# Performance work log

Measured on AMD Instinct MI355X. Metric: run time of the kernel, lower is better.

The kernel has to match this reference:

```python
import jax, jax.numpy as jnp
import numpy as np

META_DIM, CIN, COUT, K = 32, 64, 64, 3
B, N, S = 32, 256, 64


def setup_inputs() -> dict:
    key = jax.random.key(0)
    k1, k2, k3, k4, k5, k6 = jax.random.split(key, 6)
    scale = 1.0 / np.sqrt(META_DIM)
    return {
        "meta_knowledge": jax.random.normal(k1, (B, N, META_DIM), dtype=jnp.float32),
        "x": jax.random.normal(k2, (B, N, S, CIN), dtype=jnp.float32),
        "w_lin_w": jax.random.normal(k3, (CIN * COUT * K, META_DIM), dtype=jnp.float32) * scale,
        "w_lin_b": jax.random.normal(k4, (CIN * COUT * K,), dtype=jnp.float32) * scale,
        "b_lin_w": jax.random.normal(k5, (COUT, META_DIM), dtype=jnp.float32) * scale,
        "b_lin_b": jax.random.normal(k6, (COUT,), dtype=jnp.float32) * scale,
    }


def reference(meta_knowledge, x, w_lin_w, w_lin_b, b_lin_w, b_lin_b):
    # meta_knowledge: [B, N, M]; x: [B, N, S, Cin]
    b, n, s, cin = x.shape
    cout = b_lin_w.shape[0]
    k = w_lin_w.shape[0] // (cin * cout)
    s_out = s - k + 1

    # Hypernetwork: per-(batch,node) conv weights and biases
    # w: [B, N, Cout, Cin, K]
    w = (jnp.einsum("bnm,pm->bnp", meta_knowledge, w_lin_w) + w_lin_b)
    w = w.reshape(b, n, cout, cin, k)
    # bias: [B, N, Cout]
    bias = jnp.einsum("bnm,om->bno", meta_knowledge, b_lin_w) + b_lin_b

    # Sliding windows over seq axis (valid conv): [B, N, S_out, K, Cin]
    x_win = jnp.stack([x[:, :, j : j + s_out, :] for j in range(k)], axis=3)

    # Per-group dynamic conv as batched contraction: [B, N, S_out, Cout]
    out = jnp.einsum("bntkc,bnock->bnto", x_win, w) + bias[:, :, None, :]
    return out
```

## Files before the change

### kernel.cpp

```cpp
#include <hip/hip_runtime.h>
#include <hip/hip_bf16.h>


#define BN_TOT   8192
#define C_IN     64
#define C_OUT    64
#define M_DIM    32
#define S_OUT    62

#define NT       8
#define NTHREADS 1024
#define OSTR     104
#define WNODE    (16 * OSTR + 8)
#define WBUF     (NT * WNODE)
#define WLW_ROWS 12288
#define WS_NEED  (WLW_ROWS * M_DIM * 2 + WLW_ROWS * 4)

typedef __attribute__((ext_vector_type(8))) short bf16x8;
typedef __attribute__((ext_vector_type(4))) float f32x4;

static __device__ __forceinline__ short f2bf(float f) {
    return __bfloat16_as_short(__float2bfloat16(f));
}

static __device__ __forceinline__ bf16x8 cvt8(float4 a, float4 b) {
    bf16x8 r;
    r[0] = f2bf(a.x); r[1] = f2bf(a.y); r[2] = f2bf(a.z); r[3] = f2bf(a.w);
    r[4] = f2bf(b.x); r[5] = f2bf(b.y); r[6] = f2bf(b.z); r[7] = f2bf(b.w);
    return r;
}

extern "C" __global__ void wlw_to_bf16(const float* __restrict__ src,
                                       short* __restrict__ dst) {
    const int i = (blockIdx.x * 256 + threadIdx.x) * 8;
    const float4 a = *reinterpret_cast<const float4*>(src + i);
    const float4 b = *reinterpret_cast<const float4*>(src + i + 4);
    *reinterpret_cast<bf16x8*>(dst + i) = cvt8(a, b);
}

extern "C" __global__ void wlb_rearr(const float* __restrict__ wlb,
                                     float* __restrict__ wlbR) {
    const int i = blockIdx.x * 256 + threadIdx.x;
    const int o = i / 192;
    const int r = i - o * 192;
    const int k = r >> 6;
    const int c = r & 63;
    wlbR[i] = wlb[o * 192 + c * 3 + k];
}

template <int USE_WS>
__global__ void __launch_bounds__(NTHREADS, 4)
metaconv_fused(const float* __restrict__ meta,
               const float* __restrict__ x,
               const float* __restrict__ wlw,
               const short* __restrict__ wlwbf,
               const float* __restrict__ wlb,
               const float* __restrict__ wlbR,
               const float* __restrict__ blw,
               const float* __restrict__ blb,
               float* __restrict__ out)
{
    __shared__ short wsh[2 * WBUF];
    __shared__ float bias_s[NT][C_OUT];

    const int tid   = threadIdx.x;
    const int wave  = tid >> 6;
    const int lane  = tid & 63;
    const int l16   = lane & 15;
    const int g     = lane >> 4;
    const int node  = wave & (NT - 1);
    const int thalf = wave >> 3;
    const int bn0   = blockIdx.x * NT;

    const float* xsrc = x + (size_t)(bn0 + node) * (64 * C_IN);

    if (tid < NT * C_OUT) {
        const int bnode = tid >> 6;
        const int o     = tid & 63;
        const float* mrow = meta + (size_t)(bn0 + bnode) * M_DIM;
        const float* brow = blw + o * M_DIM;
        float s = blb[o];
        #pragma unroll
        for (int m = 0; m < M_DIM; ++m) s += mrow[m] * brow[m];
        bias_s[bnode][o] = s;
    }

    bf16x8 metaF;
    {
        const float* mp = meta + (size_t)(bn0 + (l16 & (NT - 1))) * M_DIM + g * 8;
        metaF = cvt8(*reinterpret_cast<const float4*>(mp),
                     *reinterpret_cast<const float4*>(mp + 4));
    }

    bf16x8 Abf[2][3];
    auto load_A = [&](int c0) {
        #pragma unroll
        for (int ttl = 0; ttl < 2; ++ttl) {
            float4 ra[3], rb[3];
            #pragma unroll
            for (int k = 0; k < 3; ++k) {
                int row = thalf * 32 + ttl * 16 + l16 + k;
                row = row < 63 ? row : 63;
                const float* p = xsrc + row * 64 + c0 + g * 8;
                ra[k] = *reinterpret_cast<const float4*>(p);
                rb[k] = *reinterpret_cast<const float4*>(p + 4);
            }
            #pragma unroll
            for (int k = 0; k < 3; ++k) Abf[ttl][k] = cvt8(ra[k], rb[k]);
        }
    };

    auto hyper = [&](int c0, int oq, int buf) {
        const int og = oq * 16 + wave;
        short* wd = wsh + buf * WBUF;
        #pragma unroll
        for (int ch = 0; ch < 2; ++ch) {
            #pragma unroll
            for (int k = 0; k < 3; ++k) {
                const int pr = og * 192 + (c0 + ch * 16 + l16) * 3 + k;
                bf16x8 aF;
                f32x4 Cf;
                if constexpr (USE_WS) {
                    aF = *reinterpret_cast<const bf16x8*>(wlwbf + (size_t)pr * M_DIM + g * 8);
                    const float4 cf = *reinterpret_cast<const float4*>(
                        wlbR + (og * 3 + k) * 64 + c0 + ch * 16 + g * 4);
                    Cf[0] = cf.x; Cf[1] = cf.y; Cf[2] = cf.z; Cf[3] = cf.w;
                } else {
                    const float* wp = wlw + (size_t)pr * M_DIM + g * 8;
                    aF = cvt8(*reinterpret_cast<const float4*>(wp),
                              *reinterpret_cast<const float4*>(wp + 4));
                    const int cb = c0 + ch * 16 + g * 4;
                    const int pb = og * 192 + k;
                    Cf[0] = wlb[pb + (cb + 0) * 3];
                    Cf[1] = wlb[pb + (cb + 1) * 3];
                    Cf[2] = wlb[pb + (cb + 2) * 3];
                    Cf[3] = wlb[pb + (cb + 3) * 3];
                }
                const f32x4 d = __builtin_amdgcn_mfma_f32_16x16x32_bf16(aF, metaF, Cf, 0, 0, 0);
                if (l16 < NT) {
                    const int off = l16 * WNODE + wave * OSTR + k * 32 + ch * 16 + g * 4;
                    *reinterpret_cast<short4*>(&wd[off]) =
                        make_short4(f2bf(d[0]), f2bf(d[1]), f2bf(d[2]), f2bf(d[3]));
                }
            }
        }
    };

    const f32x4 ZV = {0.f, 0.f, 0.f, 0.f};
    f32x4 acc[2][4];
    #pragma unroll
    for (int t = 0; t < 2; ++t)
        #pragma unroll
        for (int o = 0; o < 4; ++o) acc[t][o] = ZV;

    load_A(0);
    hyper(0, 0, 0);
    __syncthreads();

    #pragma unroll
    for (int cc = 0; cc < 2; ++cc) {
        #pragma unroll
        for (int oq = 0; oq < 4; ++oq) {
            const int P = cc * 4 + oq;
            if (P == 4) load_A(32);
            if (P < 7) {
                const int Pn = P + 1;
                hyper((Pn >> 2) * 32, Pn & 3, Pn & 1);
            }
            const short* wn = wsh + (P & 1) * WBUF + node * WNODE;
            bf16x8 B[3];
            #pragma unroll
            for (int k = 0; k < 3; ++k)
                B[k] = *reinterpret_cast<const bf16x8*>(wn + l16 * OSTR + k * 32 + g * 8);
            #pragma unroll
            for (int ttl = 0; ttl < 2; ++ttl)
                #pragma unroll
                for (int k = 0; k < 3; ++k)
                    acc[ttl][oq] = __builtin_amdgcn_mfma_f32_16x16x32_bf16(
                        Abf[ttl][k], B[k], acc[ttl][oq], 0, 0, 0);
            __syncthreads();
        }
    }

    float* ob = out + (size_t)(bn0 + node) * (S_OUT * C_OUT);
    #pragma unroll
    for (int ttl = 0; ttl < 2; ++ttl) {
        #pragma unroll
        for (int ot = 0; ot < 4; ++ot) {
            const int o  = ot * 16 + l16;
            const float bv = bias_s[node][o];
            #pragma unroll
            for (int r = 0; r < 4; ++r) {
                const int t = thalf * 32 + ttl * 16 + g * 4 + r;
                if (t < S_OUT) ob[t * C_OUT + o] = acc[ttl][ot][r] + bv;
            }
        }
    }
}

extern "C" void kernel_launch(void* const* d_in, const int* in_sizes, int n_in,
                              void* d_out, int out_size, void* d_ws, size_t ws_size,
                              hipStream_t stream) {
    const float* meta = (const float*)d_in[0];
    const float* x    = (const float*)d_in[1];
    const float* wlw  = (const float*)d_in[2];
    const float* wlb  = (const float*)d_in[3];
    const float* blw  = (const float*)d_in[4];
    const float* blb  = (const float*)d_in[5];
    float* out = (float*)d_out;
    (void)in_sizes; (void)n_in; (void)out_size;

    short* wlwbf = (short*)d_ws;
    float* wlbR  = (float*)((char*)d_ws + (size_t)WLW_ROWS * M_DIM * 2);

    if (ws_size >= (size_t)WS_NEED) {
        wlw_to_bf16<<<dim3(WLW_ROWS * M_DIM / (256 * 8)), dim3(256), 0, stream>>>(wlw, wlwbf);
        wlb_rearr<<<dim3(WLW_ROWS / 256), dim3(256), 0, stream>>>(wlb, wlbR);
        metaconv_fused<1><<<dim3(BN_TOT / NT), dim3(NTHREADS), 0, stream>>>(
            meta, x, wlw, wlwbf, wlb, wlbR, blw, blb, out);
    } else {
        metaconv_fused<0><<<dim3(BN_TOT / NT), dim3(NTHREADS), 0, stream>>>(
            meta, x, wlw, wlwbf, wlb, wlbR, blw, blb, out);
    }
}
```

Measured before the change: 165.7 us.

## Split hypernetwork weight generation into separate kernel writing bf16 weights to workspace

Replaces the fused kernel, which regenerated per-node conv weights inside the conv loop, with two kernels. The first materializes bf16 per-node weights in a workspace, chunked to fit the workspace size. The second streams those weights through double-buffered registers into LDS and convolves against x, which is staged once into swizzled LDS. This removes hypernetwork MFMA work from the conv kernel at the cost of writing and reading about 200 MB of intermediate weights through HBM plus extra launches. The fallback fused kernel also stages x in LDS.

```diff
diff --git a/kernel.cpp b/kernel.cpp
--- a/kernel.cpp
+++ b/kernel.cpp
@@ -7,14 +7,11 @@
 #define C_OUT    64
 #define M_DIM    32
 #define S_OUT    62
-
-#define NT       8
-#define NTHREADS 1024
-#define OSTR     104
-#define WNODE    (16 * OSTR + 8)
-#define WBUF     (NT * WNODE)
 #define WLW_ROWS 12288
-#define WS_NEED  (WLW_ROWS * M_DIM * 2 + WLW_ROWS * 4)
+
+#define OSTR2    200
+#define NODE_W   12800
+#define A_NPAD   1608
 
 typedef __attribute__((ext_vector_type(8))) short bf16x8;
 typedef __attribute__((ext_vector_type(4))) float f32x4;
@@ -48,33 +45,137 @@
     wlbR[i] = wlb[o * 192 + c * 3 + k];
 }
 
-template <int USE_WS>
-__global__ void __launch_bounds__(NTHREADS, 4)
-metaconv_fused(const float* __restrict__ meta,
-               const float* __restrict__ x,
-               const float* __restrict__ wlw,
-               const short* __restrict__ wlwbf,
-               const float* __restrict__ wlb,
-               const float* __restrict__ wlbR,
-               const float* __restrict__ blw,
-               const float* __restrict__ blb,
-               float* __restrict__ out)
+extern "C" __global__ void __launch_bounds__(512, 4)
+hyper_write_w(const float* __restrict__ meta,
+              const short* __restrict__ wlwbf,
+              const float* __restrict__ wlbR,
+              short* __restrict__ W,
+              int bn_base)
 {
-    __shared__ short wsh[2 * WBUF];
-    __shared__ float bias_s[NT][C_OUT];
+    __shared__ short st[16 * A_NPAD];
+
+    const int tid  = threadIdx.x;
+    const int wave = tid >> 6;
+    const int lane = tid & 63;
+    const int l16  = lane & 15;
+    const int g    = lane >> 4;
+    const int bn0  = bn_base + blockIdx.x * 16;
+    const int og0  = blockIdx.y * 8;
+    const int og   = og0 + wave;
+
+    bf16x8 metaF;
+    {
+        const float* mp = meta + (size_t)(bn0 + l16) * M_DIM + g * 8;
+        metaF = cvt8(*reinterpret_cast<const float4*>(mp),
+                     *reinterpret_cast<const float4*>(mp + 4));
+    }
+
+    #pragma unroll 1
+    for (int cp = 0; cp < 2; ++cp) {
+        #pragma unroll
+        for (int ci = 0; ci < 2; ++ci) {
+            const int ch4 = cp * 2 + ci;
+            #pragma unroll
+            for (int k = 0; k < 3; ++k) {
+                const int c  = ch4 * 16 + l16;
+                const int pr = og * 192 + c * 3 + k;
+                const bf16x8 aF = *reinterpret_cast<const bf16x8*>(
+                    wlwbf + (size_t)pr * M_DIM + g * 8);
+                const float4 cf = *reinterpret_cast<const float4*>(
+                    wlbR + (og * 3 + k) * 64 + ch4 * 16 + g * 4);
+                f32x4 Cf; Cf[0] = cf.x; Cf[1] = cf.y; Cf[2] = cf.z; Cf[3] = cf.w;
+                const f32x4 d = __builtin_amdgcn_mfma_f32_16x16x32_bf16(aF, metaF, Cf, 0, 0, 0);
+                const int off = l16 * A_NPAD + wave * OSTR2 + k * 64 + ch4 * 16 + g * 4;
+                *reinterpret_cast<short4*>(&st[off]) =
+                    make_short4(f2bf(d[0]), f2bf(d[1]), f2bf(d[2]), f2bf(d[3]));
+            }
+        }
+    }
+    __syncthreads();
+
+    const size_t wb = (size_t)(blockIdx.x * 16) * NODE_W + (size_t)og0 * OSTR2;
+    #pragma unroll
+    for (int i = 0; i < 7; ++i) {
+        const int u = i * 512 + tid;
+        if (u < 3200) {
+            const int nd = u / 200;
+            const int rc = u - nd * 200;
+            const int4 v = *reinterpret_cast<const int4*>(&st[nd * A_NPAD + rc * 8]);
+            *reinterpret_cast<int4*>(W + wb + (size_t)nd * NODE_W + rc * 8) = v;
+        }
+    }
+}
+
+#define B_DYN  ((32768 + 25600) * 2)
+
+extern "C" __global__ void __launch_bounds__(1024, 4)
+conv_stream(const float* __restrict__ meta,
+            const float* __restrict__ x,
+            const short* __restrict__ W,
+            const float* __restrict__ blw,
+            const float* __restrict__ blb,
+            float* __restrict__ out,
+            int bn_base)
+{
+    extern __shared__ __align__(16) short dynsm[];
+    short* xsh = dynsm;
+    short* wsh = dynsm + 32768;
+    __shared__ float bias_s[8][C_OUT];
 
     const int tid   = threadIdx.x;
     const int wave  = tid >> 6;
     const int lane  = tid & 63;
     const int l16   = lane & 15;
     const int g     = lane >> 4;
-    const int node  = wave & (NT - 1);
+    const int node  = wave & 7;
     const int thalf = wave >> 3;
-    const int bn0   = blockIdx.x * NT;
-
-    const float* xsrc = x + (size_t)(bn0 + node) * (64 * C_IN);
-
-    if (tid < NT * C_OUT) {
+    const int ln0   = blockIdx.x * 8;
+    const int bn0   = bn_base + ln0;
+
+    int4 wr[2][4];
+    auto load_w = [&](int q, int s) {
+        #pragma unroll
+        for (int i = 0; i < 4; ++i) {
+            const int u = i * 1024 + tid;
+            if (u < 3200) {
+                const int nd = u / 400;
+                const int rc = u - nd * 400;
+                wr[s][i] = *reinterpret_cast<const int4*>(
+                    W + (size_t)(ln0 + nd) * NODE_W + q * 3200 + rc * 8);
+            }
+        }
+    };
+    auto write_w = [&](int s) {
+        #pragma unroll
+        for (int i = 0; i < 4; ++i) {
+            const int u = i * 1024 + tid;
+            if (u < 3200) {
+                const int nd = u / 400;
+                const int rc = u - nd * 400;
+                *reinterpret_cast<int4*>(wsh + nd * 3200 + rc * 8) = wr[s][i];
+            }
+        }
+    };
+
+    load_w(0, 0);
+
+    {
+        const float* xsrc = x + (size_t)(bn0 + node) * (64 * C_IN);
+        short* xd = xsh + node * 4096;
+        const int ts0 = thalf * 32;
+        #pragma unroll
+        for (int i = 0; i < 4; ++i) {
+            const int gi = i * 64 + lane;
+            const int tl = ts0 + (gi >> 3);
+            const int gr = gi & 7;
+            const float4 a = *reinterpret_cast<const float4*>(xsrc + tl * 64 + gr * 8);
+            const float4 b = *reinterpret_cast<const float4*>(xsrc + tl * 64 + gr * 8 + 4);
+            const int so = (gr * 8) ^ ((tl & 7) << 3);
+            *reinterpret_cast<bf16x8*>(xd + tl * 64 + so) = cvt8(a, b);
+        }
+    }
+
+    if (tid < 8 * C_OUT) {
         const int bnode = tid >> 6;
         const int o     = tid & 63;
         const float* mrow = meta + (size_t)(bn0 + bnode) * M_DIM;
@@ -85,67 +186,140 @@
         bias_s[bnode][o] = s;
     }
 
+    const f32x4 ZV = {0.f, 0.f, 0.f, 0.f};
+    f32x4 acc[2][4];
+    #pragma unroll
+    for (int t = 0; t < 2; ++t)
+        #pragma unroll
+        for (int o = 0; o < 4; ++o) acc[t][o] = ZV;
+
+    write_w(0);
+    __syncthreads();
+
+    #pragma unroll
+    for (int q = 0; q < 4; ++q) {
+        if (q < 3) load_w(q + 1, (q + 1) & 1);
+
+        const short* wn = wsh + node * 3200;
+        const short* xn = xsh + node * 4096;
+        bf16x8 B[2][3];
+        #pragma unroll
+        for (int cc2 = 0; cc2 < 2; ++cc2)
+            #pragma unroll
+            for (int k = 0; k < 3; ++k)
+                B[cc2][k] = *reinterpret_cast<const bf16x8*>(
+                    wn + l16 * OSTR2 + k * 64 + cc2 * 32 + g * 8);
+        #pragma unroll
+        for (int ttl = 0; ttl < 2; ++ttl) {
+            #pragma unroll
+            for (int cc2 = 0; cc2 < 2; ++cc2) {
+                #pragma unroll
+                for (int k = 0; k < 3; ++k) {
+                    int row = thalf * 32 + ttl * 16 + l16 + k;
+                    row = row < 63 ? row : 63;
+                    const int so = (cc2 * 32 + g * 8) ^ ((row & 7) << 3);
+                    const bf16x8 A = *reinterpret_cast<const bf16x8*>(
+                        xn + row * 64 + so);
+                    acc[ttl][q] = __builtin_amdgcn_mfma_f32_16x16x32_bf16(
+                        A, B[cc2][k], acc[ttl][q], 0, 0, 0);
+                }
+            }
+        }
+        __syncthreads();
+        if (q < 3) {
+            write_w((q + 1) & 1);
+            __syncthreads();
+        }
+    }
+
+    float* ob = out + (size_t)(bn0 + node) * (S_OUT * C_OUT);
+    #pragma unroll
+    for (int ttl = 0; ttl < 2; ++ttl) {
+        #pragma unroll
+        for (int ot = 0; ot < 4; ++ot) {
+            const int o  = ot * 16 + l16;
+            const float bv = bias_s[node][o];
+            #pragma unroll
+            for (int r = 0; r < 4; ++r) {
+                const int t = thalf * 32 + ttl * 16 + g * 4 + r;
+                if (t < S_OUT) ob[t * C_OUT + o] = acc[ttl][ot][r] + bv;
+            }
+        }
+    }
+}
+
+#define OSTRF    104
+#define WNODEF   (16 * OSTRF + 8)
+#define WBUFF    (8 * WNODEF)
+
+extern "C" __global__ void __launch_bounds__(1024, 4)
+metaconv_fused_nows(const float* __restrict__ meta, const float* __restrict__ x,
+                    const float* __restrict__ wlw, const float* __restrict__ wlb,
+                    const float* __restrict__ blw, const float* __restrict__ blb,
+                    float* __restrict__ out)
+{
+    __shared__ short wsh[2 * WBUFF];
+    __shared__ short xshf[8 * 4096];
+    __shared__ float bias_s[8][C_OUT];
+
+    const int tid = threadIdx.x, wave = tid >> 6, lane = tid & 63;
+    const int l16 = lane & 15, g = lane >> 4;
+    const int node = wave & 7, thalf = wave >> 3;
+    const int bn0 = blockIdx.x * 8;
+
+    {
+        const float* xsrc = x + (size_t)(bn0 + node) * (64 * C_IN);
+        short* xd = xshf + node * 4096;
+        const int ts0 = thalf * 32;
+        #pragma unroll
+        for (int i = 0; i < 4; ++i) {
+            const int gi = i * 64 + lane;
+            const int tl = ts0 + (gi >> 3), gr = gi & 7;
+            const float4 a = *reinterpret_cast<const float4*>(xsrc + tl * 64 + gr * 8);
+            const float4 b = *reinterpret_cast<const float4*>(xsrc + tl * 64 + gr * 8 + 4);
+            const int so = (gr * 8) ^ ((tl & 7) << 3);
+            *reinterpret_cast<bf16x8*>(xd + tl * 64 + so) = cvt8(a, b);
+        }
+    }
+    if (tid < 8 * C_OUT) {
+        const int bnode = tid >> 6, o = tid & 63;
+        const float* mrow = meta + (size_t)(bn0 + bnode) * M_DIM;
+        const float* brow = blw + o * M_DIM;
+        float s = blb[o];
+        #pragma unroll
+        for (int m = 0; m < M_DIM; ++m) s += mrow[m] * brow[m];
+        bias_s[bnode][o] = s;
+    }
     bf16x8 metaF;
     {
-        const float* mp = meta + (size_t)(bn0 + (l16 & (NT - 1))) * M_DIM + g * 8;
+        const float* mp = meta + (size_t)(bn0 + (l16 & 7)) * M_DIM + g * 8;
         metaF = cvt8(*reinterpret_cast<const float4*>(mp),
                      *reinterpret_cast<const float4*>(mp + 4));
     }
-
-    bf16x8 Abf[2][3];
-    auto load_A = [&](int c0) {
-        #pragma unroll
-        for (int ttl = 0; ttl < 2; ++ttl) {
-            float4 ra[3], rb[3];
-            #pragma unroll
-            for (int k = 0; k < 3; ++k) {
-                int row = thalf * 32 + ttl * 16 + l16 + k;
-                row = row < 63 ? row : 63;
-                const float* p = xsrc + row * 64 + c0 + g * 8;
-                ra[k] = *reinterpret_cast<const float4*>(p);
-                rb[k] = *reinterpret_cast<const float4*>(p + 4);
-            }
-            #pragma unroll
-            for (int k = 0; k < 3; ++k) Abf[ttl][k] = cvt8(ra[k], rb[k]);
-        }
-    };
-
     auto hyper = [&](int c0, int oq, int buf) {
         const int og = oq * 16 + wave;
-        short* wd = wsh + buf * WBUF;
+        short* wd = wsh + buf * WBUFF;
         #pragma unroll
         for (int ch = 0; ch < 2; ++ch) {
             #pragma unroll
             for (int k = 0; k < 3; ++k) {
                 const int pr = og * 192 + (c0 + ch * 16 + l16) * 3 + k;
-                bf16x8 aF;
+                const float* wp = wlw + (size_t)pr * M_DIM + g * 8;
+                const bf16x8 aF = cvt8(*reinterpret_cast<const float4*>(wp),
+                                       *reinterpret_cast<const float4*>(wp + 4));
+                const int cb = c0 + ch * 16 + g * 4, pb = og * 192 + k;
                 f32x4 Cf;
-                if constexpr (USE_WS) {
-                    aF = *reinterpret_cast<const bf16x8*>(wlwbf + (size_t)pr * M_DIM + g * 8);
-                    const float4 cf = *reinterpret_cast<const float4*>(
-                        wlbR + (og * 3 + k) * 64 + c0 + ch * 16 + g * 4);
-                    Cf[0] = cf.x; Cf[1] = cf.y; Cf[2] = cf.z; Cf[3] = cf.w;
-                } else {
-                    const float* wp = wlw + (size_t)pr * M_DIM + g * 8;
-                    aF = cvt8(*reinterpret_cast<const float4*>(wp),
-                              *reinterpret_cast<const float4*>(wp + 4));
-                    const int cb = c0 + ch * 16 + g * 4;
-                    const int pb = og * 192 + k;
-                    Cf[0] = wlb[pb + (cb + 0) * 3];
-                    Cf[1] = wlb[pb + (cb + 1) * 3];
-                    Cf[2] = wlb[pb + (cb + 2) * 3];
-                    Cf[3] = wlb[pb + (cb + 3) * 3];
-                }
+                Cf[0] = wlb[pb + (cb + 0) * 3]; Cf[1] = wlb[pb + (cb + 1) * 3];
+                Cf[2] = wlb[pb + (cb + 2) * 3]; Cf[3] = wlb[pb + (cb + 3) * 3];
                 const f32x4 d = __builtin_amdgcn_mfma_f32_16x16x32_bf16(aF, metaF, Cf, 0, 0, 0);
-                if (l16 < NT) {
-                    const int off = l16 * WNODE + wave * OSTR + k * 32 + ch * 16 + g * 4;
+                if (l16 < 8) {
+                    const int off = l16 * WNODEF + wave * OSTRF + k * 32 + ch * 16 + g * 4;
                     *reinterpret_cast<short4*>(&wd[off]) =
                         make_short4(f2bf(d[0]), f2bf(d[1]), f2bf(d[2]), f2bf(d[3]));
                 }
             }
         }
     };
-
     const f32x4 ZV = {0.f, 0.f, 0.f, 0.f};
     f32x4 acc[2][4];
     #pragma unroll
@@ -153,41 +327,40 @@
         #pragma unroll
         for (int o = 0; o < 4; ++o) acc[t][o] = ZV;
 
-    load_A(0);
     hyper(0, 0, 0);
     __syncthreads();
-
     #pragma unroll
     for (int cc = 0; cc < 2; ++cc) {
         #pragma unroll
         for (int oq = 0; oq < 4; ++oq) {
             const int P = cc * 4 + oq;
-            if (P == 4) load_A(32);
-            if (P < 7) {
-                const int Pn = P + 1;
-                hyper((Pn >> 2) * 32, Pn & 3, Pn & 1);
-            }
-            const short* wn = wsh + (P & 1) * WBUF + node * WNODE;
+            if (P < 7) hyper(((P + 1) >> 2) * 32, (P + 1) & 3, (P + 1) & 1);
+            const short* wn = wsh + (P & 1) * WBUFF + node * WNODEF;
+            const short* xn = xshf + node * 4096;
             bf16x8 B[3];
             #pragma unroll
             for (int k = 0; k < 3; ++k)
-                B[k] = *reinterpret_cast<const bf16x8*>(wn + l16 * OSTR + k * 32 + g * 8);
+                B[k] = *reinterpret_cast<const bf16x8*>(wn + l16 * OSTRF + k * 32 + g * 8);
             #pragma unroll
             for (int ttl = 0; ttl < 2; ++ttl)
                 #pragma unroll
-                for (int k = 0; k < 3; ++k)
+                for (int k = 0; k < 3; ++k) {
+                    int row = thalf * 32 + ttl * 16 + l16 + k;
+                    row = row < 63 ? row : 63;
+                    const int so = (cc * 32 + g * 8) ^ ((row & 7) << 3);
+                    const bf16x8 A = *reinterpret_cast<const bf16x8*>(xn + row * 64 + so);
                     acc[ttl][oq] = __builtin_amdgcn_mfma_f32_16x16x32_bf16(
-                        Abf[ttl][k], B[k], acc[ttl][oq], 0, 0, 0);
+                        A, B[k], acc[ttl][oq], 0, 0, 0);
+                }
             __syncthreads();
         }
     }
-
     float* ob = out + (size_t)(bn0 + node) * (S_OUT * C_OUT);
     #pragma unroll
-    for (int ttl = 0; ttl < 2; ++ttl) {
+    for (int ttl = 0; ttl < 2; ++ttl)
         #pragma unroll
         for (int ot = 0; ot < 4; ++ot) {
-            const int o  = ot * 16 + l16;
+            const int o = ot * 16 + l16;
             const float bv = bias_s[node][o];
             #pragma unroll
             for (int r = 0; r < 4; ++r) {
@@ -195,7 +368,6 @@
                 if (t < S_OUT) ob[t * C_OUT + o] = acc[ttl][ot][r] + bv;
             }
         }
-    }
 }
 
 extern "C" void kernel_launch(void* const* d_in, const int* in_sizes, int n_in,
@@ -210,16 +382,29 @@
     float* out = (float*)d_out;
     (void)in_sizes; (void)n_in; (void)out_size;
 
-    short* wlwbf = (short*)d_ws;
-    float* wlbR  = (float*)((char*)d_ws + (size_t)WLW_ROWS * M_DIM * 2);
-
-    if (ws_size >= (size_t)WS_NEED) {
+    const size_t fixed = (size_t)WLW_ROWS * M_DIM * 2 + (size_t)WLW_ROWS * 4;
+    int nchunk = 0;
+    for (int n = 1; n <= 8; n *= 2) {
+        if (ws_size >= fixed + (size_t)(BN_TOT / n) * NODE_W * 2) { nchunk = n; break; }
+    }
+
+    if (nchunk) {
+        short* wlwbf = (short*)d_ws;
+        float* wlbR  = (float*)((char*)d_ws + (size_t)WLW_ROWS * M_DIM * 2);
+        short* Warea = (short*)((char*)d_ws + fixed);
+        (void)hipFuncSetAttribute((const void*)&conv_stream,
+                                  hipFuncAttributeMaxDynamicSharedMemorySize, B_DYN);
         wlw_to_bf16<<<dim3(WLW_ROWS * M_DIM / (256 * 8)), dim3(256), 0, stream>>>(wlw, wlwbf);
         wlb_rearr<<<dim3(WLW_ROWS / 256), dim3(256), 0, stream>>>(wlb, wlbR);
-        metaconv_fused<1><<<dim3(BN_TOT / NT), dim3(NTHREADS), 0, stream>>>(
-            meta, x, wlw, wlwbf, wlb, wlbR, blw, blb, out);
+        const int nodes = BN_TOT / nchunk;
+        for (int c = 0; c < nchunk; ++c) {
+            hyper_write_w<<<dim3(nodes / 16, 8), dim3(512), 0, stream>>>(
+                meta, wlwbf, wlbR, Warea, c * nodes);
+            conv_stream<<<dim3(nodes / 8), dim3(1024), B_DYN, stream>>>(
+                meta, x, Warea, blw, blb, out, c * nodes);
+        }
     } else {
-        metaconv_fused<0><<<dim3(BN_TOT / NT), dim3(NTHREADS), 0, stream>>>(
-            meta, x, wlw, wlwbf, wlb, wlbR, blw, blb, out);
-    }
-}
+        metaconv_fused_nows<<<dim3(BN_TOT / 8), dim3(1024), 0, stream>>>(
+            meta, x, wlw, wlb, blw, blb, out);
+    }
+}
```

After: 218.6 us. 31.9% more time.
